# Performance work log

Hardware: AMD Instinct MI355X
Metric: run time of the kernel (lower is better)

Reference implementation:

```python
import jax, jax.numpy as jnp
import numpy as np

EPS = 1e-5
TEMP = 50.0


def setup_inputs() -> dict:
    key = jax.random.key(0)
    features = jax.random.normal(key, (4, 64, 128, 128), dtype=jnp.float32)
    return {"features": features, "patch_sim_neiref_neisimavgsize": 5}


def reference(features, patch_sim_neiref_neisimavgsize):
    k = patch_sim_neiref_neisimavgsize
    B, C, H, W = features.shape
    pad = k // 2
    xp = jnp.pad(features, ((0, 0), (0, 0), (pad, pad), (pad, pad)))
    # windows ordered (kh, kw) to match F.unfold: [B, k*k, C, H, W]
    wins = jnp.stack([xp[:, :, i:i + H, j:j + W]
                      for i in range(k) for j in range(k)], axis=1)
    # [B, H, W, k*k, C]
    patch = jnp.transpose(wins, (0, 3, 4, 1, 2)) + EPS
    patch_norm = patch / jnp.sqrt(jnp.sum(patch * patch, axis=-1, keepdims=True))
    center = patch_norm[..., (k * k) // 2:(k * k) // 2 + 1, :]  # center pixel of window
    sim = jnp.sum(patch_norm * center, axis=-1, keepdims=True)   # cosine sim [B,H,W,kk,1]
    wei = jax.nn.softmax(TEMP * sim, axis=-2)
    repr_vec = jnp.sum(patch * wei, axis=-2)                     # [B,H,W,C]
    return jnp.transpose(repr_vec, (0, 3, 1, 2))                 # [B,C,H,W]
```

## Files before the change

### kernel.cpp

```cpp
#include <hip/hip_runtime.h>

#define EPS 1e-5f
#define TEMP 50.0f
#define CCH 64
#define HH 128
#define WW 128
#define HWSZ (HH * WW)
#define CEPS2 (CCH * EPS * EPS)

#define IT 8
#define HT 12
#define HPX (HT * HT)
#define HPAD 145

typedef _Float16 h16;
typedef h16 h2v __attribute__((ext_vector_type(2)));
typedef h16 h8v __attribute__((ext_vector_type(8)));
union H8 { h8v v; h2v p[4]; };

__device__ __forceinline__ float fdot2(h2v a, h2v b, float c) {
#if __has_builtin(__builtin_amdgcn_fdot2)
    return __builtin_amdgcn_fdot2(a, b, c, false);
#else
    return c + (float)a[0] * (float)b[0] + (float)a[1] * (float)b[1];
#endif
}

__global__ __launch_bounds__(128) void rv_fused(const float* __restrict__ x,
                                                float* __restrict__ out) {
    __shared__ h8v  tile[8][HPAD];
    __shared__ float sh_q[HPX];

    const int t  = threadIdx.x;
    const int w0 = blockIdx.x * IT;
    const int h0 = blockIdx.y * IT;
    const int b  = blockIdx.z;
    const float* xb = x + (size_t)b * (CCH * HWSZ);

#pragma unroll
    for (int it = 0; it < 9; ++it) {
        int k = it * 128 + t;
        int hq = k / HPX;
        int px = k - hq * HPX;
        int row = px / HT;
        int col = px - row * HT;
        int gh = h0 + row - 2;
        int gw = w0 + col - 2;
        float vv[8] = {0.f, 0.f, 0.f, 0.f, 0.f, 0.f, 0.f, 0.f};
        if (gh >= 0 && gh < HH && gw >= 0 && gw < WW) {
            const float* p = xb + (size_t)(hq * 8) * HWSZ + gh * WW + gw;
#pragma unroll
            for (int j = 0; j < 8; ++j) vv[j] = p[j * HWSZ];
        }
        h8v hv;
#pragma unroll
        for (int j = 0; j < 8; ++j) hv[j] = (h16)vv[j];
        tile[hq][px] = hv;
    }
    __syncthreads();

    for (int idx = t; idx < HPX; idx += 128) {
        float q = 0.f;
#pragma unroll
        for (int hq = 0; hq < 8; ++hq) {
            H8 u; u.v = tile[hq][idx];
#pragma unroll
            for (int j = 0; j < 4; ++j) q = fdot2(u.p[j], u.p[j], q);
        }
        sh_q[idx] = q;
    }

    const int half = t & 1;
    const int pix  = t >> 1;
    const int r    = pix >> 3;
    const int c    = pix & 7;
    const int cpx  = (r + 2) * HT + (c + 2);

    H8 ctr[4];
#pragma unroll
    for (int g = 0; g < 4; ++g) ctr[g].v = tile[4 * half + g][cpx];

    float D[25];
#pragma unroll
    for (int dr = 0; dr < 5; ++dr) {
#pragma unroll
        for (int dc = 0; dc < 5; ++dc) {
            const int npx = (r + dr) * HT + (c + dc);
            float d = 0.f;
#pragma unroll
            for (int g = 0; g < 4; ++g) {
                H8 a; a.v = tile[4 * half + g][npx];
#pragma unroll
                for (int j = 0; j < 4; ++j) d = fdot2(ctr[g].p[j], a.p[j], d);
            }
            D[dr * 5 + dc] = d;
        }
    }
#pragma unroll
    for (int n = 0; n < 25; ++n) D[n] += __shfl_xor(D[n], 1);

    __syncthreads();

    const float N2c = sh_q[cpx] + CEPS2;
    float lg[25];
    float m = -1e30f;
#pragma unroll
    for (int dr = 0; dr < 5; ++dr) {
#pragma unroll
        for (int dc = 0; dc < 5; ++dc) {
            const int n = dr * 5 + dc;
            const int npx = (r + dr) * HT + (c + dc);
            const float N2n = sh_q[npx] + CEPS2;
            const float sim = (D[n] + CEPS2) * rsqrtf(N2n * N2c);
            lg[n] = TEMP * sim;
            m = fmaxf(m, lg[n]);
        }
    }
    float wei[25];
    float sum = 0.f;
#pragma unroll
    for (int n = 0; n < 25; ++n) {
        wei[n] = __expf(lg[n] - m);
        sum += wei[n];
    }
    const float rs = 1.f / sum;
#pragma unroll
    for (int n = 0; n < 25; ++n) wei[n] *= rs;

    float acc[32];
#pragma unroll
    for (int j = 0; j < 32; ++j) acc[j] = EPS;
#pragma unroll
    for (int dr = 0; dr < 5; ++dr) {
#pragma unroll
        for (int dc = 0; dc < 5; ++dc) {
            const int npx = (r + dr) * HT + (c + dc);
            const float wn = wei[dr * 5 + dc];
#pragma unroll
            for (int g = 0; g < 4; ++g) {
                H8 a; a.v = tile[4 * half + g][npx];
#pragma unroll
                for (int j = 0; j < 8; ++j)
                    acc[g * 8 + j] = fmaf(wn, (float)a.v[j], acc[g * 8 + j]);
            }
        }
    }

    const size_t obase = (size_t)b * (CCH * HWSZ)
                       + (size_t)(32 * half) * HWSZ
                       + (h0 + r) * WW + (w0 + c);
#pragma unroll
    for (int j = 0; j < 32; ++j) {
        out[obase + (size_t)j * HWSZ] = acc[j];
    }
}

extern "C" void kernel_launch(void* const* d_in, const int* in_sizes, int n_in,
                              void* d_out, int out_size, void* d_ws, size_t ws_size,
                              hipStream_t stream) {
    const float* x = (const float*)d_in[0];
    float* outp = (float*)d_out;
    rv_fused<<<dim3(WW / IT, HH / IT, 4), dim3(128, 1, 1), 0, stream>>>(x, outp);
}
```

Before: 90.54 us.

## Pre-transpose input to fp16 NHWC and accumulate weighted sum in packed fp16

Adds a pre-pass kernel that converts the NCHW fp32 input into an fp16 channel-last buffer in the workspace. The main kernel can then load each halo pixel's 8-channel group as one 16-byte vector instead of eight strided scalar loads. The weighted-sum accumulation also switches from fp32 FMAs to packed fp16 multiply-adds, halving the ALU work and the accumulator registers. In exchange it adds a second launch and a full read-write of the input, and accumulating in fp16 over 25 terms lowers precision.

```diff
diff --git a/kernel.cpp b/kernel.cpp
--- a/kernel.cpp
+++ b/kernel.cpp
@@ -26,7 +26,34 @@
 #endif
 }
 
-__global__ __launch_bounds__(128) void rv_fused(const float* __restrict__ x,
+#define TP_PAD 72
+__global__ __launch_bounds__(256) void rv_transpose(const float* __restrict__ x,
+                                                    h16* __restrict__ xt) {
+    __shared__ h16 buf[WW][TP_PAD];
+    const int t = threadIdx.x;
+    const int h = blockIdx.x;
+    const int b = blockIdx.y;
+    const float* src = x + (size_t)b * (CCH * HWSZ) + h * WW;
+#pragma unroll 8
+    for (int i = 0; i < 32; ++i) {
+        int k = i * 256 + t;
+        int c = k >> 7;
+        int w = k & 127;
+        buf[w][c] = (h16)src[(size_t)c * HWSZ + w];
+    }
+    __syncthreads();
+    h16* dst = xt + (size_t)(b * HH + h) * WW * CCH;
+#pragma unroll
+    for (int j = 0; j < 4; ++j) {
+        int idx = j * 256 + t;
+        int w = idx >> 3;
+        int q = idx & 7;
+        h8v v = *(const h8v*)&buf[w][q * 8];
+        *(h8v*)&dst[(size_t)w * CCH + q * 8] = v;
+    }
+}
+
+__global__ __launch_bounds__(128) void rv_fused(const h16* __restrict__ xt,
                                                 float* __restrict__ out) {
     __shared__ h8v  tile[8][HPAD];
     __shared__ float sh_q[HPX];
@@ -35,27 +62,21 @@
     const int w0 = blockIdx.x * IT;
     const int h0 = blockIdx.y * IT;
     const int b  = blockIdx.z;
-    const float* xb = x + (size_t)b * (CCH * HWSZ);
 
 #pragma unroll
     for (int it = 0; it < 9; ++it) {
         int k = it * 128 + t;
-        int hq = k / HPX;
-        int px = k - hq * HPX;
+        int q  = k & 7;
+        int px = k >> 3;
         int row = px / HT;
         int col = px - row * HT;
         int gh = h0 + row - 2;
         int gw = w0 + col - 2;
-        float vv[8] = {0.f, 0.f, 0.f, 0.f, 0.f, 0.f, 0.f, 0.f};
+        h8v v = {};
         if (gh >= 0 && gh < HH && gw >= 0 && gw < WW) {
-            const float* p = xb + (size_t)(hq * 8) * HWSZ + gh * WW + gw;
-#pragma unroll
-            for (int j = 0; j < 8; ++j) vv[j] = p[j * HWSZ];
+            v = *(const h8v*)&xt[((size_t)(b * HH + gh) * WW + gw) * CCH + q * 8];
         }
-        h8v hv;
-#pragma unroll
-        for (int j = 0; j < 8; ++j) hv[j] = (h16)vv[j];
-        tile[hq][px] = hv;
+        tile[q][px] = v;
     }
     __syncthreads();
 
@@ -127,21 +148,22 @@
 #pragma unroll
     for (int n = 0; n < 25; ++n) wei[n] *= rs;
 
-    float acc[32];
+    h2v acc2[16];
 #pragma unroll
-    for (int j = 0; j < 32; ++j) acc[j] = EPS;
+    for (int i = 0; i < 16; ++i) acc2[i] = (h2v){(h16)0.f, (h16)0.f};
 #pragma unroll
     for (int dr = 0; dr < 5; ++dr) {
 #pragma unroll
         for (int dc = 0; dc < 5; ++dc) {
             const int npx = (r + dr) * HT + (c + dc);
-            const float wn = wei[dr * 5 + dc];
+            const h16 wh = (h16)wei[dr * 5 + dc];
+            const h2v w2 = {wh, wh};
 #pragma unroll
             for (int g = 0; g < 4; ++g) {
                 H8 a; a.v = tile[4 * half + g][npx];
 #pragma unroll
-                for (int j = 0; j < 8; ++j)
-                    acc[g * 8 + j] = fmaf(wn, (float)a.v[j], acc[g * 8 + j]);
+                for (int j = 0; j < 4; ++j)
+                    acc2[g * 4 + j] = a.p[j] * w2 + acc2[g * 4 + j];
             }
         }
     }
@@ -150,8 +172,9 @@
                        + (size_t)(32 * half) * HWSZ
                        + (h0 + r) * WW + (w0 + c);
 #pragma unroll
-    for (int j = 0; j < 32; ++j) {
-        out[obase + (size_t)j * HWSZ] = acc[j];
+    for (int i = 0; i < 16; ++i) {
+        out[obase + (size_t)(2 * i) * HWSZ]     = (float)acc2[i][0] + EPS;
+        out[obase + (size_t)(2 * i + 1) * HWSZ] = (float)acc2[i][1] + EPS;
     }
 }
 
@@ -160,5 +183,8 @@
                               hipStream_t stream) {
     const float* x = (const float*)d_in[0];
     float* outp = (float*)d_out;
-    rv_fused<<<dim3(WW / IT, HH / IT, 4), dim3(128, 1, 1), 0, stream>>>(x, outp);
+    h16* xt = (h16*)d_ws;
+
+    rv_transpose<<<dim3(HH, 4), dim3(256), 0, stream>>>(x, xt);
+    rv_fused<<<dim3(WW / IT, HH / IT, 4), dim3(128, 1, 1), 0, stream>>>(xt, outp);
 }
```

Result: faster. 83.79 us (-7.5%).
